# Performance work log

Hardware: AMD Instinct MI355X
Metric: run time of the kernel (lower is better)

Reference implementation:

```python
import jax, jax.numpy as jnp
import numpy as np

H = 8          # kv heads
D = 128        # head dim
EPS = 1e-6
NEG = -1e9

def rmsnorm(x, w):
    rms = jnp.sqrt(jnp.mean(x * x, axis=-1, keepdims=True) + EPS)
    return x / rms * w

def apply_rotary(x, cos, sin):
    # x: [B, h, T, D]; cos/sin: [1, 1, T, D/2]
    x1, x2 = jnp.split(x, 2, axis=-1)
    return jnp.concatenate([x1 * cos - x2 * sin, x1 * sin + x2 * cos], axis=-1)


def setup_inputs() -> dict:
    key = jax.random.key(0)
    ks = jax.random.split(key, 7)
    B, T, hid = 1, 4096, 1024
    s = 0.02
    return {
        "x":   jax.random.normal(ks[0], (B, T, hid), jnp.float32),
        "cos": jax.random.normal(ks[1], (1, 1, T, D // 2), jnp.float32),
        "sin": jax.random.normal(ks[2], (1, 1, T, D // 2), jnp.float32),
        "Wq":  jax.random.normal(ks[3], (hid, 2 * hid), jnp.float32) * s,
        "Wk":  jax.random.normal(ks[4], (hid, hid), jnp.float32) * s,
        "Wv":  jax.random.normal(ks[5], (hid, hid), jnp.float32) * s,
        "Wo":  jax.random.normal(ks[6], (2 * hid, hid), jnp.float32) * s,
        "qn_w": jnp.ones((D,), jnp.float32),
        "kn_w": jnp.ones((D,), jnp.float32),
    }


def reference(x, cos, sin, Wq, Wk, Wv, Wo, qn_w, kn_w):
    B, T, _ = x.shape
    scale = D ** -0.5

    q = (x @ Wq).reshape(B, T, 2 * H, D).transpose(0, 2, 1, 3)  # [B,2H,T,D]
    k = (x @ Wk).reshape(B, T, H, D).transpose(0, 2, 1, 3)      # [B,H,T,D]
    v = (x @ Wv).reshape(B, T, H, D).transpose(0, 2, 1, 3)      # [B,H,T,D]

    q = apply_rotary(rmsnorm(q, qn_w), cos, sin)
    k = apply_rotary(rmsnorm(k, kn_w), cos, sin)

    # GQA expand: query head i uses kv head i // 2
    k = jnp.repeat(k, 2, axis=1)  # [B,2H,T,D]
    v = jnp.repeat(v, 2, axis=1)

    attn = jnp.einsum("bhtd,bhsd->bhts", q, k) * scale
    causal = jnp.tril(jnp.ones((T, T), bool))
    attn = jnp.where(causal, attn, NEG)
    attn = jax.nn.softmax(attn, axis=-1)

    out = jnp.einsum("bhts,bhsd->bhtd", attn, v)
    out = out.transpose(0, 2, 1, 3).reshape(B, T, 2 * H * D)
    return out @ Wo
```

## Files before the change

kernel.cpp:

```cpp
#include <hip/hip_runtime.h>
#include <hip/hip_bf16.h>

#define H2 16
#define HKV 8
#define DHEAD 128
#define HID 1024
#define NQ 2048

typedef unsigned short u16;
typedef __bf16 bf16x8 __attribute__((ext_vector_type(8)));
typedef float f32x4 __attribute__((ext_vector_type(4)));

__device__ __forceinline__ u16 f2bf(float x) {
    unsigned int u = __float_as_uint(x);
    unsigned int r = (u + 0x7fffu + ((u >> 16) & 1u)) >> 16;
    return (u16)r;
}
__device__ __forceinline__ float bf2f(u16 x) {
    return __uint_as_float(((unsigned int)x) << 16);
}

__device__ __forceinline__ unsigned int pack_bf16(float hi, float lo) {
    unsigned int a = __float_as_uint(hi) + 0x8000u;
    unsigned int b = __float_as_uint(lo) + 0x8000u;
    return __builtin_amdgcn_perm(a, b, 0x07060302u);
}

__device__ __forceinline__ bf16x8 ld_frag(const u16* p) {
    bf16x8 r;
    *reinterpret_cast<uint4*>(&r) = *reinterpret_cast<const uint4*>(p);
    return r;
}

__device__ __forceinline__ void gload_lds16(const u16* g, u16* l) {
    __builtin_amdgcn_global_load_lds((const __attribute__((address_space(1))) void*)g,
                                     (__attribute__((address_space(3))) void*)l, 16, 0, 0);
}

__global__ __launch_bounds__(256) void cast_f32_bf16(const float* __restrict__ in,
                                                     u16* __restrict__ out, int n4) {
    int i = blockIdx.x * 256 + threadIdx.x;
    if (i < n4) {
        float4 v = reinterpret_cast<const float4*>(in)[i];
        ushort4 o;
        o.x = f2bf(v.x); o.y = f2bf(v.y); o.z = f2bf(v.z); o.w = f2bf(v.w);
        reinterpret_cast<ushort4*>(out)[i] = o;
    }
}

__global__ __launch_bounds__(256) void transpose_cast_all(const float* __restrict__ Wq,
                                                          const float* __restrict__ Wk,
                                                          const float* __restrict__ Wv,
                                                          const float* __restrict__ Wo,
                                                          u16* __restrict__ Wqkvb,
                                                          u16* __restrict__ Wob) {
    __shared__ u16 t[32][34];
    int bid = blockIdx.x;
    const float* in; u16* out; int K, N, k0, n0;
    if (bid < 2048) {
        in = Wq; out = Wqkvb; K = 1024; N = 2048;
        k0 = (bid & 31) * 32; n0 = (bid >> 5) * 32;
    } else if (bid < 3072) {
        int b = bid - 2048;
        in = Wk; out = Wqkvb + (size_t)2048 * 1024; K = 1024; N = 1024;
        k0 = (b & 31) * 32; n0 = (b >> 5) * 32;
    } else if (bid < 4096) {
        int b = bid - 3072;
        in = Wv; out = Wqkvb + (size_t)3072 * 1024; K = 1024; N = 1024;
        k0 = (b & 31) * 32; n0 = (b >> 5) * 32;
    } else {
        int b = bid - 4096;
        in = Wo; out = Wob; K = 2048; N = 1024;
        k0 = (b & 63) * 32; n0 = (b >> 6) * 32;
    }
    for (int c = threadIdx.x; c < 1024; c += 256) {
        int k = c >> 5, n = c & 31;
        t[k][n] = f2bf(in[(size_t)(k0 + k) * N + n0 + n]);
    }
    __syncthreads();
    for (int c = threadIdx.x; c < 1024; c += 256) {
        int n = c >> 5, k = c & 31;
        out[(size_t)(n0 + n) * K + k0 + k] = t[k][n];
    }
}

template <bool OUT_BF16>
__global__ __launch_bounds__(256) void gemm_bf16_t(const u16* __restrict__ A,
                                                   const u16* __restrict__ Bt,
                                                   void* __restrict__ Cv,
                                                   int M, int N, int K) {
    __shared__ u16 As[2][128 * 32];
    __shared__ u16 Bs[2][128 * 32];
    int tid = threadIdx.x;
    int lane = tid & 63, wave = tid >> 6;
    int quad = lane >> 4, l15 = lane & 15;
    int wr = wave >> 1, wc = wave & 1;
    int m0 = blockIdx.y * 128, n0 = blockIdx.x * 128;

    f32x4 zero = {0.f, 0.f, 0.f, 0.f};
    f32x4 acc[4][4];
    for (int i = 0; i < 4; i++)
        for (int j = 0; j < 4; j++) acc[i][j] = zero;

    int r0 = 16 * wave + (lane >> 2);
    int r1 = r0 + 64;
    int ks0 = (lane & 3) ^ ((r0 >> 1) & 3);
    int ks1 = (lane & 3) ^ ((r1 >> 1) & 3);
    const u16* ga0 = A + (size_t)(m0 + r0) * K + ks0 * 8;
    const u16* ga1 = A + (size_t)(m0 + r1) * K + ks1 * 8;
    const u16* gb0 = Bt + (size_t)(n0 + r0) * K + ks0 * 8;
    const u16* gb1 = Bt + (size_t)(n0 + r1) * K + ks1 * 8;

    int swz = (quad ^ ((l15 >> 1) & 3)) * 8;

    for (int k0 = 0; k0 < K; k0 += 64) {
        __syncthreads();
        #pragma unroll
        for (int s = 0; s < 2; s++) {
            gload_lds16(ga0 + k0 + s * 32, &As[s][wave * 512]);
            gload_lds16(ga1 + k0 + s * 32, &As[s][(wave + 4) * 512]);
            gload_lds16(gb0 + k0 + s * 32, &Bs[s][wave * 512]);
            gload_lds16(gb1 + k0 + s * 32, &Bs[s][(wave + 4) * 512]);
        }
        __syncthreads();
        #pragma unroll
        for (int s = 0; s < 2; s++) {
            bf16x8 a[4], b[4];
            #pragma unroll
            for (int i = 0; i < 4; i++) a[i] = ld_frag(&As[s][(64 * wr + 16 * i + l15) * 32 + swz]);
            #pragma unroll
            for (int j = 0; j < 4; j++) b[j] = ld_frag(&Bs[s][(64 * wc + 16 * j + l15) * 32 + swz]);
            #pragma unroll
            for (int i = 0; i < 4; i++)
                #pragma unroll
                for (int j = 0; j < 4; j++)
                    acc[i][j] = __builtin_amdgcn_mfma_f32_16x16x32_bf16(a[i], b[j], acc[i][j], 0, 0, 0);
        }
    }
    for (int i = 0; i < 4; i++) {
        int rowb = m0 + 64 * wr + 16 * i + quad * 4;
        for (int j = 0; j < 4; j++) {
            int col = n0 + 64 * wc + 16 * j + l15;
            for (int r = 0; r < 4; r++) {
                if (OUT_BF16)
                    ((u16*)Cv)[(size_t)(rowb + r) * N + col] = f2bf(acc[i][j][r]);
                else
                    ((float*)Cv)[(size_t)(rowb + r) * N + col] = acc[i][j][r];
            }
        }
    }
}

__global__ __launch_bounds__(256) void gemm_bf16_n64(const u16* __restrict__ A,
                                                     const u16* __restrict__ Bt,
                                                     float* __restrict__ C,
                                                     int M, int N, int K) {
    __shared__ u16 As[2][128 * 32];
    __shared__ u16 Bs[2][64 * 32];
    int tid = threadIdx.x;
    int lane = tid & 63, wave = tid >> 6;
    int quad = lane >> 4, l15 = lane & 15;
    int m0 = blockIdx.y * 128, n0 = blockIdx.x * 64;

    f32x4 zero = {0.f, 0.f, 0.f, 0.f};
    f32x4 acc[2][4];
    for (int i = 0; i < 2; i++)
        for (int j = 0; j < 4; j++) acc[i][j] = zero;

    int ra0 = 32 * wave + (lane >> 2);
    int ra1 = ra0 + 16;
    int rb  = 16 * wave + (lane >> 2);
    int ksa0 = (lane & 3) ^ ((ra0 >> 1) & 3);
    int ksa1 = (lane & 3) ^ ((ra1 >> 1) & 3);
    int ksb  = (lane & 3) ^ ((rb >> 1) & 3);
    const u16* ga0 = A + (size_t)(m0 + ra0) * K + ksa0 * 8;
    const u16* ga1 = A + (size_t)(m0 + ra1) * K + ksa1 * 8;
    const u16* gb  = Bt + (size_t)(n0 + rb) * K + ksb * 8;

    int swz = (quad ^ ((l15 >> 1) & 3)) * 8;

    for (int k0 = 0; k0 < K; k0 += 64) {
        __syncthreads();
        #pragma unroll
        for (int s = 0; s < 2; s++) {
            gload_lds16(ga0 + k0 + s * 32, &As[s][(2 * wave) * 512]);
            gload_lds16(ga1 + k0 + s * 32, &As[s][(2 * wave + 1) * 512]);
            gload_lds16(gb + k0 + s * 32, &Bs[s][wave * 512]);
        }
        __syncthreads();
        #pragma unroll
        for (int s = 0; s < 2; s++) {
            bf16x8 a[2], b[4];
            #pragma unroll
            for (int i = 0; i < 2; i++) a[i] = ld_frag(&As[s][(32 * wave + 16 * i + l15) * 32 + swz]);
            #pragma unroll
            for (int j = 0; j < 4; j++) b[j] = ld_frag(&Bs[s][(16 * j + l15) * 32 + swz]);
            #pragma unroll
            for (int i = 0; i < 2; i++)
                #pragma unroll
                for (int j = 0; j < 4; j++)
                    acc[i][j] = __builtin_amdgcn_mfma_f32_16x16x32_bf16(a[i], b[j], acc[i][j], 0, 0, 0);
        }
    }
    for (int i = 0; i < 2; i++) {
        int rowb = m0 + 32 * wave + 16 * i + quad * 4;
        for (int j = 0; j < 4; j++) {
            int col = n0 + 16 * j + l15;
            for (int r = 0; r < 4; r++)
                C[(size_t)(rowb + r) * N + col] = acc[i][j][r];
        }
    }
}

__global__ __launch_bounds__(256) void norm_rope_qk(const u16* __restrict__ qkv,
                                                    const float* __restrict__ cosp,
                                                    const float* __restrict__ sinp,
                                                    const float* __restrict__ qnw,
                                                    const float* __restrict__ knw,
                                                    u16* __restrict__ Qb,
                                                    u16* __restrict__ Kb,
                                                    int T, float qscale) {
    int wave = threadIdx.x >> 6, lane = threadIdx.x & 63;
    int wid = blockIdx.x * 4 + wave;
    int t = wid / 24, unit = wid % 24;
    if (t >= T) return;
    bool isq = unit < 16;
    int coloff = isq ? unit * 128 : 2048 + (unit - 16) * 128;
    const float* w = isq ? qnw : knw;
    float outscale = isq ? qscale : 1.0f;
    u16* out = isq ? (Qb + ((size_t)unit * T + t) * 128)
                   : (Kb + ((size_t)(unit - 16) * T + t) * 128);
    const u16* r = qkv + (size_t)t * 4096 + coloff;
    float v1 = bf2f(r[lane]), v2 = bf2f(r[lane + 64]);
    float ss = v1 * v1 + v2 * v2;
    for (int off = 1; off < 64; off <<= 1) ss += __shfl_xor(ss, off);
    float inv = rsqrtf(ss * (1.f / 128.f) + 1e-6f);
    float n1 = v1 * inv * w[lane], n2 = v2 * inv * w[lane + 64];
    float c = cosp[(size_t)t * 64 + lane], s = sinp[(size_t)t * 64 + lane];
    float o1 = (n1 * c - n2 * s) * outscale;
    float o2 = (n1 * s + n2 * c) * outscale;
    out[lane] = f2bf(o1);
    out[lane + 64] = f2bf(o2);
}

__global__ __launch_bounds__(256) void v_transpose(const u16* __restrict__ qkv,
                                                   u16* __restrict__ Vbt, int T) {
    __shared__ u16 tt[128][72];
    int h = blockIdx.y, t0 = blockIdx.x * 64;
    for (int c = threadIdx.x; c < 8192; c += 256) {
        int r = c >> 7, d = c & 127;
        tt[d][r] = qkv[(size_t)(t0 + r) * 4096 + 3072 + h * 128 + d];
    }
    __syncthreads();
    for (int c = threadIdx.x; c < 8192; c += 256) {
        int d = c >> 6, r = c & 63;
        Vbt[((size_t)h * 128 + d) * T + t0 + r] = tt[d][r];
    }
}

__global__ __launch_bounds__(256) void flash_attn(const u16* __restrict__ Qb,
                                                  const u16* __restrict__ Kb,
                                                  const u16* __restrict__ Vbt,
                                                  u16* __restrict__ attn, int T) {
    __shared__ u16 Ks[2][64 * 128];
    __shared__ u16 Vt[2][128 * 64];
    __shared__ u16 Ps[64 * 64];
    int tid = threadIdx.x;
    int lane = tid & 63, wave = tid >> 6;
    int quad = lane >> 4, l15 = lane & 15;
    int swb8 = (l15 & 7) * 8;
    int h = blockIdx.y;
    int j = (int)blockIdx.x;
    int kvh = h >> 1;

    const u16* kbase = Kb + (size_t)kvh * T * 128;
    const u16* vbase = Vbt + (size_t)kvh * 128 * T;

    int krow_ = (lane >> 4);
    int kseg_ = (lane & 15);
    int vrow_ = (lane >> 3);
    int vseg_ = (lane & 7);

    auto stage = [&](int s0, int b) {
        #pragma unroll
        for (int i = 0; i < 4; i++) {
            int ch = wave * 4 + i;
            int r = ch * 4 + krow_;
            int s = kseg_ ^ (r & 7);
            gload_lds16(kbase + (size_t)(s0 + r) * 128 + s * 8, &Ks[b][ch * 512]);
        }
        #pragma unroll
        for (int i = 0; i < 4; i++) {
            int ch = wave * 4 + i;
            int d = ch * 8 + vrow_;
            int s = vseg_ ^ (d & 7);
            gload_lds16(vbase + (size_t)d * T + s0 + s * 8, &Vt[b][ch * 512]);
        }
    };

    bf16x8 onesf;
    #pragma unroll
    for (int i = 0; i < 8; i++) onesf[i] = (__bf16)1.0f;
    f32x4 zero = {0.f, 0.f, 0.f, 0.f};
    const float L2E = 1.44269504f;

    for (int pass = 0; pass < 2; ++pass) {
        int qt = pass == 0 ? (63 - j) : j;
        int q0 = qt * 64;

        bf16x8 qf[4];
        {
            const u16* qp = Qb + ((size_t)h * T + q0 + 16 * wave + l15) * 128 + quad * 8;
            #pragma unroll
            for (int kk = 0; kk < 4; kk++) qf[kk] = ld_frag(qp + kk * 32);
        }

        float m_i = -3.0e38f;
        f32x4 lsum = zero;
        f32x4 o[8];
        for (int dt = 0; dt < 8; dt++) o[dt] = zero;

        int ntiles = qt + 1;
        stage(0, 0);
        __syncthreads();

        for (int it = 0; it < ntiles; ++it) {
            int b = it & 1;
            if (it + 1 < ntiles) stage((it + 1) * 64, 1 - b);
            int s0 = it * 64;

            f32x4 scT[4];
            for (int jt = 0; jt < 4; jt++) scT[jt] = zero;
            #pragma unroll
            for (int kk = 0; kk < 4; kk++)
                #pragma unroll
                for (int jt = 0; jt < 4; jt++) {
                    bf16x8 kfrag = ld_frag(&Ks[b][(jt * 16 + l15) * 128 + ((kk * 32 + quad * 8) ^ swb8)]);
                    scT[jt] = __builtin_amdgcn_mfma_f32_16x16x32_bf16(kfrag, qf[kk], scT[jt], 0, 0, 0);
                }

            if (s0 == q0) {
                int qloc = 16 * wave + l15;
                #pragma unroll
                for (int jt = 0; jt < 4; jt++)
                    for (int r = 0; r < 4; r++)
                        if (jt * 16 + quad * 4 + r > qloc) scT[jt][r] = -1e30f;
            }

            float mt = scT[0][0];
            #pragma unroll
            for (int jt = 0; jt < 4; jt++)
                for (int r = 0; r < 4; r++) mt = fmaxf(mt, scT[jt][r]);
            mt = fmaxf(mt, __shfl_xor(mt, 16));
            mt = fmaxf(mt, __shfl_xor(mt, 32));
            float mnew = fmaxf(m_i, mt);
            float alpha = __expf(m_i - mnew);
            m_i = mnew;
            float mls = mnew * L2E;

            #pragma unroll
            for (int jt = 0; jt < 4; jt++)
                for (int r = 0; r < 4; r++)
                    scT[jt][r] = exp2f(fmaf(scT[jt][r], L2E, -mls));

            {
                int prow = 16 * wave + l15;
                #pragma unroll
                for (int jt = 0; jt < 4; jt++) {
                    int s8 = 2 * jt + (quad >> 1);
                    uint2 wv;
                    wv.x = pack_bf16(scT[jt][1], scT[jt][0]);
                    wv.y = pack_bf16(scT[jt][3], scT[jt][2]);
                    *reinterpret_cast<uint2*>(&Ps[prow * 64 + (s8 ^ (l15 & 7)) * 8 + (quad & 1) * 4]) = wv;
                }
            }

            if (__any(alpha != 1.0f)) {
                float av[4];
                #pragma unroll
                for (int r = 0; r < 4; r++) av[r] = __shfl(alpha, quad * 4 + r);
                #pragma unroll
                for (int r = 0; r < 4; r++) lsum[r] *= av[r];
                #pragma unroll
                for (int dt = 0; dt < 8; dt++)
                    for (int r = 0; r < 4; r++) o[dt][r] *= av[r];
            }

            asm volatile("s_waitcnt lgkmcnt(0)" ::: "memory");

            #pragma unroll
            for (int kk2 = 0; kk2 < 2; kk2++) {
                bf16x8 pa = ld_frag(&Ps[(16 * wave + l15) * 64 + (((4 * kk2 + quad) ^ (l15 & 7)) * 8)]);
                lsum = __builtin_amdgcn_mfma_f32_16x16x32_bf16(pa, onesf, lsum, 0, 0, 0);
                #pragma unroll
                for (int dt = 0; dt < 8; dt++) {
                    bf16x8 vb = ld_frag(&Vt[b][(dt * 16 + l15) * 64 + ((kk2 * 32 + quad * 8) ^ swb8)]);
                    o[dt] = __builtin_amdgcn_mfma_f32_16x16x32_bf16(pa, vb, o[dt], 0, 0, 0);
                }
            }
            __syncthreads();
        }

        float inv[4];
        for (int r = 0; r < 4; r++) inv[r] = 1.f / lsum[r];
        for (int dt = 0; dt < 8; dt++)
            for (int r = 0; r < 4; r++) {
                int row = q0 + 16 * wave + quad * 4 + r;
                attn[(size_t)row * NQ + h * DHEAD + dt * 16 + l15] = f2bf(o[dt][r] * inv[r]);
            }
    }
}

extern "C" void kernel_launch(void* const* d_in, const int* in_sizes, int n_in,
                              void* d_out, int out_size, void* d_ws, size_t ws_size,
                              hipStream_t stream) {
    const float* x    = (const float*)d_in[0];
    const float* cosp = (const float*)d_in[1];
    const float* sinp = (const float*)d_in[2];
    const float* Wq   = (const float*)d_in[3];
    const float* Wk   = (const float*)d_in[4];
    const float* Wv   = (const float*)d_in[5];
    const float* Wo   = (const float*)d_in[6];
    const float* qnw  = (const float*)d_in[7];
    const float* knw  = (const float*)d_in[8];
    float* out = (float*)d_out;
    const int T = in_sizes[1] / 64;

    char* ws = (char*)d_ws;
    size_t off = 0;
    auto alloc = [&](size_t bytes) {
        char* p = ws + off;
        off += (bytes + 255) & ~(size_t)255;
        return p;
    };
    u16*   xb     = (u16*)alloc((size_t)T * HID * 2);
    u16*   Wqkvb  = (u16*)alloc((size_t)4096 * HID * 2);
    u16*   Wob    = (u16*)alloc((size_t)HID * NQ * 2);
    u16*   qkvb   = (u16*)alloc((size_t)T * 4096 * 2);
    u16*   Qb     = (u16*)alloc((size_t)H2 * T * DHEAD * 2);
    u16*   Kb     = (u16*)alloc((size_t)HKV * T * DHEAD * 2);
    u16*   Vbt    = (u16*)alloc((size_t)HKV * DHEAD * T * 2);
    u16*   attn   = (u16*)alloc((size_t)T * NQ * 2);

    cast_f32_bf16<<<(T * HID / 4 + 255) / 256, 256, 0, stream>>>(x, xb, T * HID / 4);
    transpose_cast_all<<<6144, 256, 0, stream>>>(Wq, Wk, Wv, Wo, Wqkvb, Wob);

    gemm_bf16_t<true><<<dim3(4096 / 128, T / 128), 256, 0, stream>>>(xb, Wqkvb, qkvb, T, 4096, HID);

    const float scale = 0.08838834764831845f;
    norm_rope_qk<<<T * 24 / 4, 256, 0, stream>>>(qkvb, cosp, sinp, qnw, knw, Qb, Kb, T, scale);
    v_transpose<<<dim3(T / 64, HKV), 256, 0, stream>>>(qkvb, Vbt, T);

    flash_attn<<<dim3(32, H2), 256, 0, stream>>>(Qb, Kb, Vbt, attn, T);

    gemm_bf16_n64<<<dim3(HID / 64, T / 128), 256, 0, stream>>>(attn, Wob, out, T, HID, NQ);
}
```

Before: 359.3 us.

## Rework flash attention to 32x32 MFMA with in-register P and split-KV waves

The flash attention kernel moves from 16x16x32 to 32x32x16 bf16 MFMA tiles. Each pair of waves now handles 32 query rows, and the two waves split the 64-key tile between them. The softmax probabilities are converted with v_cvt_pk_bf16 and rearranged across lanes with v_permlane32_swap, so P stays in registers and the shared-memory round trip for P goes away. The row sum is also computed with adds instead of an MFMA against a ones vector. The two per-wave partial results are merged at the end through LDS, which adds extra syncs and LDS traffic per pass. s_setprio is set around the MFMA sections.

```diff
diff --git a/kernel.cpp b/kernel.cpp
--- a/kernel.cpp
+++ b/kernel.cpp
@@ -10,6 +10,8 @@
 typedef unsigned short u16;
 typedef __bf16 bf16x8 __attribute__((ext_vector_type(8)));
 typedef float f32x4 __attribute__((ext_vector_type(4)));
+typedef float f32x16 __attribute__((ext_vector_type(16)));
+typedef unsigned int u32x4 __attribute__((ext_vector_type(4)));
 
 __device__ __forceinline__ u16 f2bf(float x) {
     unsigned int u = __float_as_uint(x);
@@ -20,12 +22,6 @@
     return __uint_as_float(((unsigned int)x) << 16);
 }
 
-__device__ __forceinline__ unsigned int pack_bf16(float hi, float lo) {
-    unsigned int a = __float_as_uint(hi) + 0x8000u;
-    unsigned int b = __float_as_uint(lo) + 0x8000u;
-    return __builtin_amdgcn_perm(a, b, 0x07060302u);
-}
-
 __device__ __forceinline__ bf16x8 ld_frag(const u16* p) {
     bf16x8 r;
     *reinterpret_cast<uint4*>(&r) = *reinterpret_cast<const uint4*>(p);
@@ -35,6 +31,15 @@
 __device__ __forceinline__ void gload_lds16(const u16* g, u16* l) {
     __builtin_amdgcn_global_load_lds((const __attribute__((address_space(1))) void*)g,
                                      (__attribute__((address_space(3))) void*)l, 16, 0, 0);
+}
+
+__device__ __forceinline__ unsigned int cvt_pk_bf16(float lo, float hi) {
+    unsigned int r;
+    asm("v_cvt_pk_bf16_f32 %0, %1, %2" : "=v"(r) : "v"(lo), "v"(hi));
+    return r;
+}
+__device__ __forceinline__ void swap32(unsigned int& a, unsigned int& b) {
+    asm("v_permlane32_swap_b32 %0, %1" : "+v"(a), "+v"(b));
 }
 
 __global__ __launch_bounds__(256) void cast_f32_bf16(const float* __restrict__ in,
@@ -264,11 +269,12 @@
                                                   u16* __restrict__ attn, int T) {
     __shared__ u16 Ks[2][64 * 128];
     __shared__ u16 Vt[2][128 * 64];
-    __shared__ u16 Ps[64 * 64];
+    __shared__ float Ms[2][2][32];
+    __shared__ float Ls[2][2][32];
     int tid = threadIdx.x;
     int lane = tid & 63, wave = tid >> 6;
-    int quad = lane >> 4, l15 = lane & 15;
-    int swb8 = (l15 & 7) * 8;
+    int qb = wave >> 1, sh = wave & 1;
+    int l31 = lane & 31, hi = lane >> 5;
     int h = blockIdx.y;
     int j = (int)blockIdx.x;
     int kvh = h >> 1;
@@ -276,10 +282,8 @@
     const u16* kbase = Kb + (size_t)kvh * T * 128;
     const u16* vbase = Vbt + (size_t)kvh * 128 * T;
 
-    int krow_ = (lane >> 4);
-    int kseg_ = (lane & 15);
-    int vrow_ = (lane >> 3);
-    int vseg_ = (lane & 7);
+    int krow_ = lane >> 4, kseg_ = lane & 15;
+    int vrow_ = lane >> 3, vseg_ = lane & 7;
 
     auto stage = [&](int s0, int b) {
         #pragma unroll
@@ -298,27 +302,26 @@
         }
     };
 
-    bf16x8 onesf;
-    #pragma unroll
-    for (int i = 0; i < 8; i++) onesf[i] = (__bf16)1.0f;
-    f32x4 zero = {0.f, 0.f, 0.f, 0.f};
     const float L2E = 1.44269504f;
+    int rloc = sh * 32 + l31;
 
     for (int pass = 0; pass < 2; ++pass) {
         int qt = pass == 0 ? (63 - j) : j;
         int q0 = qt * 64;
 
-        bf16x8 qf[4];
+        bf16x8 qf[8];
         {
-            const u16* qp = Qb + ((size_t)h * T + q0 + 16 * wave + l15) * 128 + quad * 8;
-            #pragma unroll
-            for (int kk = 0; kk < 4; kk++) qf[kk] = ld_frag(qp + kk * 32);
-        }
-
-        float m_i = -3.0e38f;
-        f32x4 lsum = zero;
-        f32x4 o[8];
-        for (int dt = 0; dt < 8; dt++) o[dt] = zero;
+            const u16* qp = Qb + ((size_t)h * T + q0 + qb * 32 + l31) * 128 + hi * 8;
+            #pragma unroll
+            for (int ds_ = 0; ds_ < 8; ds_++) qf[ds_] = ld_frag(qp + ds_ * 16);
+        }
+
+        float m_i = -3.0e38f, lsum = 0.f;
+        f32x16 o[4];
+        #pragma unroll
+        for (int db = 0; db < 4; db++)
+            #pragma unroll
+            for (int r = 0; r < 16; r++) o[db][r] = 0.f;
 
         int ntiles = qt + 1;
         stage(0, 0);
@@ -327,87 +330,107 @@
         for (int it = 0; it < ntiles; ++it) {
             int b = it & 1;
             if (it + 1 < ntiles) stage((it + 1) * 64, 1 - b);
-            int s0 = it * 64;
-
-            f32x4 scT[4];
-            for (int jt = 0; jt < 4; jt++) scT[jt] = zero;
-            #pragma unroll
-            for (int kk = 0; kk < 4; kk++)
-                #pragma unroll
-                for (int jt = 0; jt < 4; jt++) {
-                    bf16x8 kfrag = ld_frag(&Ks[b][(jt * 16 + l15) * 128 + ((kk * 32 + quad * 8) ^ swb8)]);
-                    scT[jt] = __builtin_amdgcn_mfma_f32_16x16x32_bf16(kfrag, qf[kk], scT[jt], 0, 0, 0);
-                }
-
-            if (s0 == q0) {
-                int qloc = 16 * wave + l15;
-                #pragma unroll
-                for (int jt = 0; jt < 4; jt++)
-                    for (int r = 0; r < 4; r++)
-                        if (jt * 16 + quad * 4 + r > qloc) scT[jt][r] = -1e30f;
-            }
-
-            float mt = scT[0][0];
-            #pragma unroll
-            for (int jt = 0; jt < 4; jt++)
-                for (int r = 0; r < 4; r++) mt = fmaxf(mt, scT[jt][r]);
-            mt = fmaxf(mt, __shfl_xor(mt, 16));
-            mt = fmaxf(mt, __shfl_xor(mt, 32));
-            float mnew = fmaxf(m_i, mt);
-            float alpha = __expf(m_i - mnew);
-            m_i = mnew;
-            float mls = mnew * L2E;
-
-            #pragma unroll
-            for (int jt = 0; jt < 4; jt++)
-                for (int r = 0; r < 4; r++)
-                    scT[jt][r] = exp2f(fmaf(scT[jt][r], L2E, -mls));
-
-            {
-                int prow = 16 * wave + l15;
-                #pragma unroll
-                for (int jt = 0; jt < 4; jt++) {
-                    int s8 = 2 * jt + (quad >> 1);
-                    uint2 wv;
-                    wv.x = pack_bf16(scT[jt][1], scT[jt][0]);
-                    wv.y = pack_bf16(scT[jt][3], scT[jt][2]);
-                    *reinterpret_cast<uint2*>(&Ps[prow * 64 + (s8 ^ (l15 & 7)) * 8 + (quad & 1) * 4]) = wv;
-                }
-            }
-
-            if (__any(alpha != 1.0f)) {
-                float av[4];
-                #pragma unroll
-                for (int r = 0; r < 4; r++) av[r] = __shfl(alpha, quad * 4 + r);
-                #pragma unroll
-                for (int r = 0; r < 4; r++) lsum[r] *= av[r];
-                #pragma unroll
-                for (int dt = 0; dt < 8; dt++)
-                    for (int r = 0; r < 4; r++) o[dt][r] *= av[r];
-            }
-
-            asm volatile("s_waitcnt lgkmcnt(0)" ::: "memory");
-
-            #pragma unroll
-            for (int kk2 = 0; kk2 < 2; kk2++) {
-                bf16x8 pa = ld_frag(&Ps[(16 * wave + l15) * 64 + (((4 * kk2 + quad) ^ (l15 & 7)) * 8)]);
-                lsum = __builtin_amdgcn_mfma_f32_16x16x32_bf16(pa, onesf, lsum, 0, 0, 0);
-                #pragma unroll
-                for (int dt = 0; dt < 8; dt++) {
-                    bf16x8 vb = ld_frag(&Vt[b][(dt * 16 + l15) * 64 + ((kk2 * 32 + quad * 8) ^ swb8)]);
-                    o[dt] = __builtin_amdgcn_mfma_f32_16x16x32_bf16(pa, vb, o[dt], 0, 0, 0);
-                }
+            bool diag = (it == qt);
+            if (!(diag && qb == 0 && sh == 1)) {
+                f32x16 sc;
+                #pragma unroll
+                for (int r = 0; r < 16; r++) sc[r] = 0.f;
+                __builtin_amdgcn_s_setprio(1);
+                #pragma unroll
+                for (int ds_ = 0; ds_ < 8; ds_++) {
+                    bf16x8 kf = ld_frag(&Ks[b][rloc * 128 + (((ds_ * 2 + hi) ^ (l31 & 7)) * 8)]);
+                    sc = __builtin_amdgcn_mfma_f32_32x32x16_bf16(kf, qf[ds_], sc, 0, 0, 0);
+                }
+                __builtin_amdgcn_s_setprio(0);
+
+                if (diag) {
+                    int qg = qb * 32 + l31;
+                    #pragma unroll
+                    for (int r = 0; r < 16; r++) {
+                        int sg = sh * 32 + (r & 3) + ((r >> 2) << 3) + (hi << 2);
+                        if (sg > qg) sc[r] = -1e30f;
+                    }
+                }
+
+                float mt = fmaxf(fmaxf(fmaxf(sc[0], sc[1]), fmaxf(sc[2], sc[3])),
+                                 fmaxf(fmaxf(sc[4], sc[5]), fmaxf(sc[6], sc[7])));
+                float mt2 = fmaxf(fmaxf(fmaxf(sc[8], sc[9]), fmaxf(sc[10], sc[11])),
+                                  fmaxf(fmaxf(sc[12], sc[13]), fmaxf(sc[14], sc[15])));
+                mt = fmaxf(mt, mt2);
+                mt = fmaxf(mt, __shfl_xor(mt, 32));
+                float mnew = fmaxf(m_i, mt);
+                float alpha = __expf(m_i - mnew);
+                m_i = mnew;
+                float mls = mnew * L2E;
+                #pragma unroll
+                for (int r = 0; r < 16; r++) sc[r] = exp2f(fmaf(sc[r], L2E, -mls));
+                float ts = ((sc[0] + sc[1]) + (sc[2] + sc[3])) + ((sc[4] + sc[5]) + (sc[6] + sc[7]));
+                ts += ((sc[8] + sc[9]) + (sc[10] + sc[11])) + ((sc[12] + sc[13]) + (sc[14] + sc[15]));
+                ts += __shfl_xor(ts, 32);
+                if (__any(alpha != 1.0f)) {
+                    lsum = fmaf(lsum, alpha, ts);
+                    #pragma unroll
+                    for (int db = 0; db < 4; db++)
+                        #pragma unroll
+                        for (int r = 0; r < 16; r++) o[db][r] *= alpha;
+                } else {
+                    lsum += ts;
+                }
+
+                __builtin_amdgcn_s_setprio(1);
+                #pragma unroll
+                for (int t2 = 0; t2 < 2; t2++) {
+                    unsigned int a0 = cvt_pk_bf16(sc[8 * t2 + 0], sc[8 * t2 + 1]);
+                    unsigned int a1 = cvt_pk_bf16(sc[8 * t2 + 4], sc[8 * t2 + 5]);
+                    unsigned int b0 = cvt_pk_bf16(sc[8 * t2 + 2], sc[8 * t2 + 3]);
+                    unsigned int b1 = cvt_pk_bf16(sc[8 * t2 + 6], sc[8 * t2 + 7]);
+                    swap32(a0, a1);
+                    swap32(b0, b1);
+                    u32x4 pw = {a0, b0, a1, b1};
+                    bf16x8 pb = *reinterpret_cast<bf16x8*>(&pw);
+                    int gD = sh * 4 + t2 * 2 + hi;
+                    #pragma unroll
+                    for (int db = 0; db < 4; db++) {
+                        int d = db * 32 + l31;
+                        bf16x8 vf = ld_frag(&Vt[b][d * 64 + ((gD ^ (d & 7)) * 8)]);
+                        o[db] = __builtin_amdgcn_mfma_f32_32x32x16_bf16(vf, pb, o[db], 0, 0, 0);
+                    }
+                }
+                __builtin_amdgcn_s_setprio(0);
             }
             __syncthreads();
         }
 
-        float inv[4];
-        for (int r = 0; r < 4; r++) inv[r] = 1.f / lsum[r];
-        for (int dt = 0; dt < 8; dt++)
-            for (int r = 0; r < 4; r++) {
-                int row = q0 + 16 * wave + quad * 4 + r;
-                attn[(size_t)row * NQ + h * DHEAD + dt * 16 + l15] = f2bf(o[dt][r] * inv[r]);
-            }
+        if (lane < 32) { Ms[qb][sh][l31] = m_i; Ls[qb][sh][l31] = lsum; }
+        __syncthreads();
+        float mo = Ms[qb][1 - sh][l31];
+        float lo_ = Ls[qb][1 - sh][l31];
+        float M = fmaxf(m_i, mo);
+        float w = __expf(m_i - M);
+        float* mbuf = reinterpret_cast<float*>(&Ks[0][0]);
+        if (sh == 1) {
+            #pragma unroll
+            for (int db = 0; db < 4; db++)
+                #pragma unroll
+                for (int r = 0; r < 16; r++) {
+                    int d = db * 32 + (r & 3) + ((r >> 2) << 3) + (hi << 2);
+                    mbuf[((size_t)qb * 128 + d) * 32 + l31] = o[db][r] * w;
+                }
+        }
+        __syncthreads();
+        if (sh == 0) {
+            float w1 = __expf(mo - M);
+            float invl = 1.f / (w * lsum + w1 * lo_);
+            #pragma unroll
+            for (int db = 0; db < 4; db++)
+                #pragma unroll
+                for (int r = 0; r < 16; r++) {
+                    int d = db * 32 + (r & 3) + ((r >> 2) << 3) + (hi << 2);
+                    float val = (o[db][r] * w + mbuf[((size_t)qb * 128 + d) * 32 + l31]) * invl;
+                    attn[(size_t)(q0 + qb * 32 + l31) * NQ + h * DHEAD + d] = f2bf(val);
+                }
+        }
+        __syncthreads();
     }
 }
 
```

New measurement: 442.6 us. 1.23x slower.

## Split KV tile across two wave groups in flash attention with merge

Applied to the files above, without the earlier changes.

Doubles the flash attention block to 512 threads. Each query-row wave is paired with a second wave that handles the other half of each 64-key tile, so each wave runs its own online softmax over 32 keys. Per-half max and sum statistics go to shared memory, and the second half's output is written to scratch in the K buffer and merged by the first wave group. This raises the number of waves per CU to hide latency, at the cost of an extra combine step, extra barriers, and higher register pressure under the new launch bounds.

```diff
diff --git a/kernel.cpp b/kernel.cpp
--- a/kernel.cpp
+++ b/kernel.cpp
@@ -258,15 +258,18 @@
     }
 }
 
-__global__ __launch_bounds__(256) void flash_attn(const u16* __restrict__ Qb,
-                                                  const u16* __restrict__ Kb,
-                                                  const u16* __restrict__ Vbt,
-                                                  u16* __restrict__ attn, int T) {
+__global__ __launch_bounds__(512, 4) void flash_attn(const u16* __restrict__ Qb,
+                                                     const u16* __restrict__ Kb,
+                                                     const u16* __restrict__ Vbt,
+                                                     u16* __restrict__ attn, int T) {
     __shared__ u16 Ks[2][64 * 128];
     __shared__ u16 Vt[2][128 * 64];
     __shared__ u16 Ps[64 * 64];
+    __shared__ float Ms[4][2][16];
+    __shared__ float Ls[4][2][16];
     int tid = threadIdx.x;
     int lane = tid & 63, wave = tid >> 6;
+    int qw = wave & 3, sh = wave >> 2;
     int quad = lane >> 4, l15 = lane & 15;
     int swb8 = (l15 & 7) * 8;
     int h = blockIdx.y;
@@ -276,22 +279,22 @@
     const u16* kbase = Kb + (size_t)kvh * T * 128;
     const u16* vbase = Vbt + (size_t)kvh * 128 * T;
 
-    int krow_ = (lane >> 4);
-    int kseg_ = (lane & 15);
-    int vrow_ = (lane >> 3);
-    int vseg_ = (lane & 7);
+    int krow_ = lane >> 4;
+    int kseg_ = lane & 15;
+    int vrow_ = lane >> 3;
+    int vseg_ = lane & 7;
 
     auto stage = [&](int s0, int b) {
         #pragma unroll
-        for (int i = 0; i < 4; i++) {
-            int ch = wave * 4 + i;
+        for (int i = 0; i < 2; i++) {
+            int ch = wave * 2 + i;
             int r = ch * 4 + krow_;
             int s = kseg_ ^ (r & 7);
             gload_lds16(kbase + (size_t)(s0 + r) * 128 + s * 8, &Ks[b][ch * 512]);
         }
         #pragma unroll
-        for (int i = 0; i < 4; i++) {
-            int ch = wave * 4 + i;
+        for (int i = 0; i < 2; i++) {
+            int ch = wave * 2 + i;
             int d = ch * 8 + vrow_;
             int s = vseg_ ^ (d & 7);
             gload_lds16(vbase + (size_t)d * T + s0 + s * 8, &Vt[b][ch * 512]);
@@ -310,7 +313,7 @@
 
         bf16x8 qf[4];
         {
-            const u16* qp = Qb + ((size_t)h * T + q0 + 16 * wave + l15) * 128 + quad * 8;
+            const u16* qp = Qb + ((size_t)h * T + q0 + 16 * qw + l15) * 128 + quad * 8;
             #pragma unroll
             for (int kk = 0; kk < 4; kk++) qf[kk] = ld_frag(qp + kk * 32);
         }
@@ -327,87 +330,121 @@
         for (int it = 0; it < ntiles; ++it) {
             int b = it & 1;
             if (it + 1 < ntiles) stage((it + 1) * 64, 1 - b);
-            int s0 = it * 64;
-
-            f32x4 scT[4];
-            for (int jt = 0; jt < 4; jt++) scT[jt] = zero;
-            #pragma unroll
-            for (int kk = 0; kk < 4; kk++)
-                #pragma unroll
-                for (int jt = 0; jt < 4; jt++) {
-                    bf16x8 kfrag = ld_frag(&Ks[b][(jt * 16 + l15) * 128 + ((kk * 32 + quad * 8) ^ swb8)]);
-                    scT[jt] = __builtin_amdgcn_mfma_f32_16x16x32_bf16(kfrag, qf[kk], scT[jt], 0, 0, 0);
+            bool diag = (it == qt);
+            if (!(diag && sh == 1 && qw < 2)) {
+                f32x4 scT[2];
+                scT[0] = zero; scT[1] = zero;
+                #pragma unroll
+                for (int kk = 0; kk < 4; kk++)
+                    #pragma unroll
+                    for (int jt = 0; jt < 2; jt++) {
+                        bf16x8 kfrag = ld_frag(&Ks[b][(sh * 32 + jt * 16 + l15) * 128 + ((kk * 32 + quad * 8) ^ swb8)]);
+                        scT[jt] = __builtin_amdgcn_mfma_f32_16x16x32_bf16(kfrag, qf[kk], scT[jt], 0, 0, 0);
+                    }
+
+                if (diag) {
+                    int qloc = 16 * qw + l15;
+                    #pragma unroll
+                    for (int jt = 0; jt < 2; jt++)
+                        for (int r = 0; r < 4; r++)
+                            if (sh * 32 + jt * 16 + quad * 4 + r > qloc) scT[jt][r] = -1e30f;
                 }
 
-            if (s0 == q0) {
-                int qloc = 16 * wave + l15;
-                #pragma unroll
-                for (int jt = 0; jt < 4; jt++)
+                float mt = scT[0][0];
+                #pragma unroll
+                for (int jt = 0; jt < 2; jt++)
+                    for (int r = 0; r < 4; r++) mt = fmaxf(mt, scT[jt][r]);
+                mt = fmaxf(mt, __shfl_xor(mt, 16));
+                mt = fmaxf(mt, __shfl_xor(mt, 32));
+                float mnew = fmaxf(m_i, mt);
+                float alpha = __expf(m_i - mnew);
+                m_i = mnew;
+                float mls = mnew * L2E;
+
+                #pragma unroll
+                for (int jt = 0; jt < 2; jt++)
                     for (int r = 0; r < 4; r++)
-                        if (jt * 16 + quad * 4 + r > qloc) scT[jt][r] = -1e30f;
-            }
-
-            float mt = scT[0][0];
-            #pragma unroll
-            for (int jt = 0; jt < 4; jt++)
-                for (int r = 0; r < 4; r++) mt = fmaxf(mt, scT[jt][r]);
-            mt = fmaxf(mt, __shfl_xor(mt, 16));
-            mt = fmaxf(mt, __shfl_xor(mt, 32));
-            float mnew = fmaxf(m_i, mt);
-            float alpha = __expf(m_i - mnew);
-            m_i = mnew;
-            float mls = mnew * L2E;
-
-            #pragma unroll
-            for (int jt = 0; jt < 4; jt++)
-                for (int r = 0; r < 4; r++)
-                    scT[jt][r] = exp2f(fmaf(scT[jt][r], L2E, -mls));
-
-            {
-                int prow = 16 * wave + l15;
-                #pragma unroll
-                for (int jt = 0; jt < 4; jt++) {
-                    int s8 = 2 * jt + (quad >> 1);
-                    uint2 wv;
-                    wv.x = pack_bf16(scT[jt][1], scT[jt][0]);
-                    wv.y = pack_bf16(scT[jt][3], scT[jt][2]);
-                    *reinterpret_cast<uint2*>(&Ps[prow * 64 + (s8 ^ (l15 & 7)) * 8 + (quad & 1) * 4]) = wv;
+                        scT[jt][r] = exp2f(fmaf(scT[jt][r], L2E, -mls));
+
+                {
+                    int prow = 16 * qw + l15;
+                    #pragma unroll
+                    for (int jt = 0; jt < 2; jt++) {
+                        int s8 = sh * 4 + 2 * jt + (quad >> 1);
+                        uint2 wv;
+                        wv.x = pack_bf16(scT[jt][1], scT[jt][0]);
+                        wv.y = pack_bf16(scT[jt][3], scT[jt][2]);
+                        *reinterpret_cast<uint2*>(&Ps[prow * 64 + (s8 ^ (l15 & 7)) * 8 + (quad & 1) * 4]) = wv;
+                    }
                 }
-            }
-
-            if (__any(alpha != 1.0f)) {
-                float av[4];
-                #pragma unroll
-                for (int r = 0; r < 4; r++) av[r] = __shfl(alpha, quad * 4 + r);
-                #pragma unroll
-                for (int r = 0; r < 4; r++) lsum[r] *= av[r];
-                #pragma unroll
-                for (int dt = 0; dt < 8; dt++)
-                    for (int r = 0; r < 4; r++) o[dt][r] *= av[r];
-            }
-
-            asm volatile("s_waitcnt lgkmcnt(0)" ::: "memory");
-
-            #pragma unroll
-            for (int kk2 = 0; kk2 < 2; kk2++) {
-                bf16x8 pa = ld_frag(&Ps[(16 * wave + l15) * 64 + (((4 * kk2 + quad) ^ (l15 & 7)) * 8)]);
+
+                if (__any(alpha != 1.0f)) {
+                    float av[4];
+                    #pragma unroll
+                    for (int r = 0; r < 4; r++) av[r] = __shfl(alpha, quad * 4 + r);
+                    #pragma unroll
+                    for (int r = 0; r < 4; r++) lsum[r] *= av[r];
+                    #pragma unroll
+                    for (int dt = 0; dt < 8; dt++)
+                        for (int r = 0; r < 4; r++) o[dt][r] *= av[r];
+                }
+
+                asm volatile("s_waitcnt lgkmcnt(0)" ::: "memory");
+
+                bf16x8 pa = ld_frag(&Ps[(16 * qw + l15) * 64 + (((sh * 4 + quad) ^ (l15 & 7)) * 8)]);
                 lsum = __builtin_amdgcn_mfma_f32_16x16x32_bf16(pa, onesf, lsum, 0, 0, 0);
                 #pragma unroll
                 for (int dt = 0; dt < 8; dt++) {
-                    bf16x8 vb = ld_frag(&Vt[b][(dt * 16 + l15) * 64 + ((kk2 * 32 + quad * 8) ^ swb8)]);
+                    bf16x8 vb = ld_frag(&Vt[b][(dt * 16 + l15) * 64 + (((sh * 4 + quad) * 8) ^ swb8)]);
                     o[dt] = __builtin_amdgcn_mfma_f32_16x16x32_bf16(pa, vb, o[dt], 0, 0, 0);
                 }
             }
             __syncthreads();
         }
 
-        float inv[4];
-        for (int r = 0; r < 4; r++) inv[r] = 1.f / lsum[r];
-        for (int dt = 0; dt < 8; dt++)
+        if (quad == 0) Ms[qw][sh][l15] = m_i;
+        if (l15 == 0) {
+            #pragma unroll
+            for (int r = 0; r < 4; r++) Ls[qw][sh][quad * 4 + r] = lsum[r];
+        }
+        __syncthreads();
+        float M4[4], wS[4];
+        #pragma unroll
+        for (int r = 0; r < 4; r++) {
+            float mS = Ms[qw][sh][quad * 4 + r];
+            float mO = Ms[qw][sh ^ 1][quad * 4 + r];
+            M4[r] = fmaxf(mS, mO);
+            wS[r] = __expf(mS - M4[r]);
+        }
+        float* scr = reinterpret_cast<float*>(&Ks[0][0]);
+        if (sh == 1) {
+            #pragma unroll
+            for (int dt = 0; dt < 8; dt++)
+                #pragma unroll
+                for (int r = 0; r < 4; r++)
+                    scr[qw * 2048 + (dt * 16 + l15) * 16 + ((quad * 4 + r) ^ l15)] = o[dt][r] * wS[r];
+        }
+        __syncthreads();
+        if (sh == 0) {
+            float inv[4];
+            #pragma unroll
             for (int r = 0; r < 4; r++) {
-                int row = q0 + 16 * wave + quad * 4 + r;
-                attn[(size_t)row * NQ + h * DHEAD + dt * 16 + l15] = f2bf(o[dt][r] * inv[r]);
+                float mO = Ms[qw][1][quad * 4 + r];
+                float wO = __expf(mO - M4[r]);
+                float l = lsum[r] * wS[r] + Ls[qw][1][quad * 4 + r] * wO;
+                inv[r] = 1.f / l;
             }
+            #pragma unroll
+            for (int dt = 0; dt < 8; dt++)
+                #pragma unroll
+                for (int r = 0; r < 4; r++) {
+                    float val = (o[dt][r] * wS[r] +
+                                 scr[qw * 2048 + (dt * 16 + l15) * 16 + ((quad * 4 + r) ^ l15)]) * inv[r];
+                    int row = q0 + 16 * qw + quad * 4 + r;
+                    attn[(size_t)row * NQ + h * DHEAD + dt * 16 + l15] = f2bf(val);
+                }
+        }
+        __syncthreads();
     }
 }
 
@@ -451,7 +488,7 @@
     norm_rope_qk<<<T * 24 / 4, 256, 0, stream>>>(qkvb, cosp, sinp, qnw, knw, Qb, Kb, T, scale);
     v_transpose<<<dim3(T / 64, HKV), 256, 0, stream>>>(qkvb, Vbt, T);
 
-    flash_attn<<<dim3(32, H2), 256, 0, stream>>>(Qb, Kb, Vbt, attn, T);
+    flash_attn<<<dim3(32, H2), 512, 0, stream>>>(Qb, Kb, Vbt, attn, T);
 
     gemm_bf16_n64<<<dim3(HID / 64, T / 128), 256, 0, stream>>>(attn, Wob, out, T, HID, NQ);
 }
```

Result: no change. 354.3 us (-1.4%).
